# Optimization experiments

Measured on AMD Instinct MI355X. Metric: run time of the kernel, lower is better.

Reference implementation:

```python
import jax, jax.numpy as jnp
import numpy as np

P = 2        # patch size (all 3 dims)
NB = 8       # num_bands
N = 16       # d_state
DTR = 8      # dt_rank = d_model // 16
DCONV = 4    # d_conv
SMAX = 2.0   # smax_dt = smax_B = smax_C


def _ln(x, g, b):
    mu = x.mean(-1, keepdims=True)
    v = ((x - mu) ** 2).mean(-1, keepdims=True)
    return (x - mu) / jnp.sqrt(v + 1e-5) * g + b


def _silu(x):
    return x * jax.nn.sigmoid(x)


def _ssm_layer(x, band, m, rho, Win, bin_, convw, convb, Wx, Wdt, bdt, Alog, Dp,
               Wout, bout, edt, eB, eC, wr, wm):
    # x: [B, L, d_model] -> bidirectional conditioned selective scan (BiFCSSM)
    Bsz, L, _ = x.shape
    ED = convw.shape[0]
    xz = x @ Win + bin_
    xp, z = xz[..., :ED], xz[..., ED:]
    # depthwise causal conv1d over L
    xpad = jnp.pad(xp, ((0, 0), (DCONV - 1, 0), (0, 0)))
    xc = sum(xpad[:, k:k + L, :] * convw[:, k] for k in range(DCONV)) + convb
    xc = _silu(xc)
    dbl = xc @ Wx                                    # [B,L,DTR+2N]
    dt = jax.nn.softplus(dbl[..., :DTR] @ Wdt + bdt)  # [B,L,ED]
    # band/radius/mask conditioned modulation of delta, B, C
    s_dt = SMAX * jax.nn.sigmoid(edt[band][None] + wr[0] * rho[None] + wm[0] * m)
    s_B = SMAX * jax.nn.sigmoid(eB[band][None] + wr[1] * rho[None] + wm[1] * m)
    s_C = SMAX * jax.nn.sigmoid(eC[band][None] + wr[2] * rho[None] + wm[2] * m)
    dt = dt * s_dt[..., None]
    Bm = dbl[..., DTR:DTR + N] * s_B[..., None]       # [B,L,N]
    Cm = dbl[..., DTR + N:] * s_C[..., None]          # [B,L,N]
    A = -jnp.exp(Alog)                                # [ED,N]
    dA = jnp.exp(dt[..., None] * A)                   # [B,L,ED,N]
    dBu = (dA - 1.0) / A * Bm[:, :, None, :] * xc[..., None]   # exact ZOH
    dA_s = jnp.moveaxis(dA, 1, 0)
    dBu_s = jnp.moveaxis(dBu, 1, 0)
    C_s = jnp.moveaxis(Cm, 1, 0)
    h0 = jnp.zeros((Bsz, ED, N), x.dtype)

    def step(h, inp):
        a, bu, c = inp
        h = a * h + bu
        return h, jnp.einsum('ben,bn->be', h, c)

    _, yf = jax.lax.scan(step, h0, (dA_s, dBu_s, C_s))
    _, yb = jax.lax.scan(step, h0, (dA_s, dBu_s, C_s), reverse=True)
    y = jnp.moveaxis(yf + yb, 0, 1) + Dp * xc
    y = y * _silu(z)
    return y @ Wout + bout


def _fwd(kspace_ri, mask, pe_w, pe_b, pu_w, pu_b, ln_g, ln_b, fn_g, fn_b,
         cond_band, cond_rad_w, cond_mask_w, l0_Win, l0_bin, l0_convw, l0_convb,
         l0_Wx, l0_Wdt, l0_bdt, l0_Alog, l0_D, l0_Wout, l0_bout, l0_edt, l0_eB,
         l0_eC, l0_wr, l0_wm):
    Bsz, C, nx, ny, nz = kspace_ri.shape
    gx, gy, gz = nx // P, ny // P, nz // P
    L = gx * gy * gz
    # patch embed (Conv3d, kernel==stride) as blocked einsum
    xr = kspace_ri.reshape(Bsz, C, gx, P, gy, P, gz, P)
    x = jnp.einsum('bcxiyjzk,dcijk->bdxyz', xr, pe_w) + pe_b[None, :, None, None, None]
    DM = x.shape[1]
    x = x.reshape(Bsz, DM, L).transpose(0, 2, 1)               # [B,L,D]
    m = mask.reshape(Bsz, 1, gx, P, gy, P, gz, P).mean(axis=(3, 5, 7)).reshape(Bsz, L)
    m = jnp.clip(m, 0.0, 1.0)
    # raster scan ordering: identity permutation, rho_bar, band ids
    rho = jnp.arange(L, dtype=x.dtype) / float(L - 1)
    band = jnp.clip(jnp.floor(rho * NB).astype(jnp.int32), 0, NB - 1)
    # condition tokens
    cond = cond_band[band][None] + rho[None, :, None] * cond_rad_w + m[:, :, None] * cond_mask_w
    h = _ln(x + cond, ln_g, ln_b)
    h = h + _ssm_layer(_ln(h, fn_g, fn_b), band, m, rho, l0_Win, l0_bin, l0_convw,
                       l0_convb, l0_Wx, l0_Wdt, l0_bdt, l0_Alog, l0_D, l0_Wout,
                       l0_bout, l0_edt, l0_eB, l0_eC, l0_wr, l0_wm)
    # patch unembed (ConvTranspose3d, kernel==stride) as blocked einsum
    hg = h.transpose(0, 2, 1).reshape(Bsz, DM, gx, gy, gz)
    out = jnp.einsum('bdxyz,dcijk->bcxiyjzk', hg, pu_w).reshape(Bsz, C, nx, ny, nz)
    out = out + pu_b[None, :, None, None, None]
    return kspace_ri + out


def setup_inputs() -> dict:
    key = jax.random.key(0)
    ks = jax.random.split(key, 24)
    ED, DM, CIN = 256, 128, 16

    def nrm(k, shape, s):
        return jax.random.normal(k, shape, jnp.float32) * s

    return {
        'kspace_ri': jax.random.normal(ks[0], (1, CIN, 64, 64, 16), jnp.float32),
        'mask': jax.random.uniform(ks[1], (1, 1, 64, 64, 16), jnp.float32),
        'pe_w': nrm(ks[2], (DM, CIN, P, P, P), 0.09),
        'pe_b': nrm(ks[3], (DM,), 0.02),
        'pu_w': nrm(ks[4], (DM, CIN, P, P, P), 0.05),
        'pu_b': jnp.zeros((CIN,), jnp.float32),
        'ln_g': jnp.ones((DM,), jnp.float32),
        'ln_b': jnp.zeros((DM,), jnp.float32),
        'fn_g': jnp.ones((DM,), jnp.float32),
        'fn_b': jnp.zeros((DM,), jnp.float32),
        'cond_band': nrm(ks[5], (NB, DM), 0.02),
        'cond_rad_w': nrm(ks[6], (DM,), 0.02),
        'cond_mask_w': nrm(ks[7], (DM,), 0.02),
        'l0_Win': nrm(ks[8], (DM, 2 * ED), 0.05),
        'l0_bin': jnp.zeros((2 * ED,), jnp.float32),
        'l0_convw': nrm(ks[9], (ED, DCONV), 0.2),
        'l0_convb': jnp.zeros((ED,), jnp.float32),
        'l0_Wx': nrm(ks[10], (ED, DTR + 2 * N), 0.05),
        'l0_Wdt': nrm(ks[11], (DTR, ED), 0.1),
        'l0_bdt': jnp.full((ED,), -3.0, jnp.float32),
        'l0_Alog': jnp.log(jnp.tile(jnp.arange(1, N + 1, dtype=jnp.float32), (ED, 1))),
        'l0_D': jnp.ones((ED,), jnp.float32),
        'l0_Wout': nrm(ks[12], (ED, DM), 0.05),
        'l0_bout': jnp.zeros((DM,), jnp.float32),
        'l0_edt': nrm(ks[13], (NB,), 0.1),
        'l0_eB': nrm(ks[14], (NB,), 0.1),
        'l0_eC': nrm(ks[15], (NB,), 0.1),
        'l0_wr': nrm(ks[16], (3,), 0.1),
        'l0_wm': nrm(ks[17], (3,), 0.1),
    }


def reference(kspace_ri, mask, pe_w, pe_b, pu_w, pu_b, ln_g, ln_b, fn_g, fn_b,
              cond_band, cond_rad_w, cond_mask_w, l0_Win, l0_bin, l0_convw,
              l0_convb, l0_Wx, l0_Wdt, l0_bdt, l0_Alog, l0_D, l0_Wout, l0_bout,
              l0_edt, l0_eB, l0_eC, l0_wr, l0_wm):
    return _fwd(kspace_ri, mask, pe_w, pe_b, pu_w, pu_b, ln_g, ln_b, fn_g, fn_b,
                cond_band, cond_rad_w, cond_mask_w, l0_Win, l0_bin, l0_convw,
                l0_convb, l0_Wx, l0_Wdt, l0_bdt, l0_Alog, l0_D, l0_Wout, l0_bout,
                l0_edt, l0_eB, l0_eC, l0_wr, l0_wm)
```

## Files before the change

### kernel.cpp

```cpp
#include <hip/hip_runtime.h>
#include <hip/hip_bf16.h>

#define L_TOK 8192
#define NCh 256
#define CLh 32

typedef short bf16x8 __attribute__((ext_vector_type(8)));
typedef float f32x4 __attribute__((ext_vector_type(4)));

static __device__ __forceinline__ ushort f2bf(float x) {
    union { float f; uint u; } v; v.f = x;
    uint r = v.u + 0x7fffu + ((v.u >> 16) & 1u);
    return (ushort)(r >> 16);
}
static __device__ __forceinline__ float bf2f(ushort h) {
    union { float f; uint u; } v; v.u = ((uint)h) << 16;
    return v.f;
}
static __device__ __forceinline__ void f2hl(float x, ushort* hi, ushort* lo) {
    ushort h = f2bf(x);
    *hi = h;
    *lo = f2bf(x - bf2f(h));
}

__global__ __launch_bounds__(256) void maskpool_k(const float* __restrict__ mask, float* __restrict__ m) {
    int l = blockIdx.x * 256 + threadIdx.x;
    int xg = l >> 8, yg = (l >> 3) & 31, zg = l & 7;
    float s = 0.f;
    for (int i2 = 0; i2 < 2; ++i2)
        for (int j2 = 0; j2 < 2; ++j2)
            for (int k2 = 0; k2 < 2; ++k2)
                s += mask[(2 * xg + i2) * 1024 + (2 * yg + j2) * 16 + 2 * zg + k2];
    s *= 0.125f;
    m[l] = fminf(fmaxf(s, 0.f), 1.f);
}

__global__ __launch_bounds__(256) void prep_w(const float* __restrict__ pe_w, const float* __restrict__ Win,
                                              const float* __restrict__ Wx, const float* __restrict__ Wout,
                                              const float* __restrict__ pu_w,
                                              ushort* __restrict__ wH, ushort* __restrict__ wL) {
    int i = blockIdx.x * 256 + threadIdx.x;
    if (i >= 147456) return;
    float v;
    if (i < 16384) {
        v = pe_w[i];
    } else if (i < 81920) {
        int j = i - 16384; int n = j >> 7, k = j & 127;
        v = Win[k * 512 + n];
    } else if (i < 98304) {
        int j = i - 81920; int n = j >> 8, k = j & 255;
        v = (n < 40) ? Wx[k * 40 + n] : 0.f;
    } else if (i < 131072) {
        int j = i - 98304; int n = j >> 8, k = j & 255;
        v = Wout[k * 128 + n];
    } else {
        int j = i - 131072; int n = j >> 7, k = j & 127;
        v = pu_w[k * 128 + n];
    }
    ushort h, lo; f2hl(v, &h, &lo);
    wH[i] = h; wL[i] = lo;
}

__global__ __launch_bounds__(256) void gather_k(const float* __restrict__ ks,
                                                ushort* __restrict__ xH, ushort* __restrict__ xL) {
    int i = blockIdx.x * 256 + threadIdx.x;
    int l = i >> 7, t = i & 127;
    int cc = t >> 3, ijk = t & 7;
    int xg = l >> 8, yg = (l >> 3) & 31, zg = l & 7;
    int i2 = (ijk >> 2) & 1, j2 = (ijk >> 1) & 1, k2 = ijk & 1;
    float v = ks[cc * 65536 + (2 * xg + i2) * 1024 + (2 * yg + j2) * 16 + 2 * zg + k2];
    ushort h, lo; f2hl(v, &h, &lo);
    xH[i] = h; xL[i] = lo;
}

template <int MODE, int K>
__global__ __launch_bounds__(256) void mgemm_k(const ushort* __restrict__ Ah, const ushort* __restrict__ Al,
                                               const ushort* __restrict__ Bh, const ushort* __restrict__ Bl,
                                               float* __restrict__ outF,
                                               ushort* __restrict__ outH, ushort* __restrict__ outL,
                                               const float* __restrict__ p0, const float* __restrict__ p1,
                                               const float* __restrict__ p2, const float* __restrict__ p3,
                                               const float* __restrict__ p4) {
    __shared__ ushort AsH[128][72], AsL[128][72];
    __shared__ ushort BsH[64][72], BsL[64][72];
    const int tid = threadIdx.x;
    const int lane = tid & 63, wave = tid >> 6;
    const int wm = wave & 1, wn = wave >> 1;
    const int ln = lane & 15, q = lane >> 4;
    const int mb = blockIdx.x * 128, nb = blockIdx.y * 64;

    f32x4 acc[4][2];
#pragma unroll
    for (int rb = 0; rb < 4; ++rb)
#pragma unroll
        for (int cb = 0; cb < 2; ++cb)
            acc[rb][cb] = (f32x4){0.f, 0.f, 0.f, 0.f};

    for (int kc = 0; kc < K; kc += 64) {
        __syncthreads();
        for (int u = tid; u < 1024; u += 256) {
            int r = u >> 3, g = u & 7;
            size_t go = (size_t)(mb + r) * K + kc + g * 8;
            *(uint4*)&AsH[r][g * 8] = *(const uint4*)&Ah[go];
            *(uint4*)&AsL[r][g * 8] = *(const uint4*)&Al[go];
        }
        for (int u = tid; u < 512; u += 256) {
            int r = u >> 3, g = u & 7;
            size_t go = (size_t)(nb + r) * K + kc + g * 8;
            *(uint4*)&BsH[r][g * 8] = *(const uint4*)&Bh[go];
            *(uint4*)&BsL[r][g * 8] = *(const uint4*)&Bl[go];
        }
        __syncthreads();
#pragma unroll
        for (int ks = 0; ks < 64; ks += 32) {
            const int kk = ks + q * 8;
            bf16x8 ah[4], al[4], bh[2], bl[2];
#pragma unroll
            for (int rb = 0; rb < 4; ++rb) {
                ah[rb] = *(const bf16x8*)&AsH[wm * 64 + rb * 16 + ln][kk];
                al[rb] = *(const bf16x8*)&AsL[wm * 64 + rb * 16 + ln][kk];
            }
#pragma unroll
            for (int cb = 0; cb < 2; ++cb) {
                bh[cb] = *(const bf16x8*)&BsH[wn * 32 + cb * 16 + ln][kk];
                bl[cb] = *(const bf16x8*)&BsL[wn * 32 + cb * 16 + ln][kk];
            }
#pragma unroll
            for (int rb = 0; rb < 4; ++rb)
#pragma unroll
                for (int cb = 0; cb < 2; ++cb) {
                    acc[rb][cb] = __builtin_amdgcn_mfma_f32_16x16x32_bf16(ah[rb], bh[cb], acc[rb][cb], 0, 0, 0);
                    acc[rb][cb] = __builtin_amdgcn_mfma_f32_16x16x32_bf16(ah[rb], bl[cb], acc[rb][cb], 0, 0, 0);
                    acc[rb][cb] = __builtin_amdgcn_mfma_f32_16x16x32_bf16(al[rb], bh[cb], acc[rb][cb], 0, 0, 0);
                }
        }
    }

#pragma unroll
    for (int rb = 0; rb < 4; ++rb) {
#pragma unroll
        for (int cb = 0; cb < 2; ++cb) {
#pragma unroll
            for (int r = 0; r < 4; ++r) {
                int l = mb + wm * 64 + rb * 16 + q * 4 + r;
                int col = nb + wn * 32 + cb * 16 + ln;
                float v = acc[rb][cb][r];
                if (MODE == 0) {
                    float rho = (float)l * (1.0f / 8191.0f);
                    int band = min(7, (int)(rho * 8.0f));
                    outF[(size_t)l * 128 + col] =
                        v + p0[col] + p1[band * 128 + col] + rho * p2[col] + p4[l] * p3[col];
                } else if (MODE == 1) {
                    outF[(size_t)l * 512 + col] = v + p0[col];
                } else if (MODE == 2) {
                    float o = v + p0[col] + p1[(size_t)l * 128 + col];
                    ushort h, lo; f2hl(o, &h, &lo);
                    outH[(size_t)l * 128 + col] = h;
                    outL[(size_t)l * 128 + col] = lo;
                } else if (MODE == 3) {
                    int xg = l >> 8, yg = (l >> 3) & 31, zg = l & 7;
                    int c = col >> 3, ijk = col & 7;
                    int i2 = (ijk >> 2) & 1, j2 = (ijk >> 1) & 1, k2 = ijk & 1;
                    size_t idx = (size_t)((c * 64 + 2 * xg + i2) * 64 + (2 * yg + j2)) * 16 + 2 * zg + k2;
                    outF[idx] = v + p0[c] + p1[idx];
                } else {
                    if (col < 40) outF[(size_t)l * 40 + col] = v;
                }
            }
        }
    }
}

__global__ __launch_bounds__(128) void ln2_k(const float* __restrict__ x,
                                             const float* __restrict__ ln_g, const float* __restrict__ ln_b,
                                             const float* __restrict__ fn_g, const float* __restrict__ fn_b,
                                             float* __restrict__ h,
                                             ushort* __restrict__ hnH, ushort* __restrict__ hnL) {
    int l = blockIdx.x, d = threadIdx.x;
    __shared__ float red[4];
    float v = x[(size_t)l * 128 + d];
    float s = v, s2 = v * v;
#pragma unroll
    for (int o = 32; o > 0; o >>= 1) { s += __shfl_xor(s, o, 64); s2 += __shfl_xor(s2, o, 64); }
    if ((d & 63) == 0) { red[d >> 6] = s; red[2 + (d >> 6)] = s2; }
    __syncthreads();
    float S = red[0] + red[1], S2 = red[2] + red[3];
    float mu = S * (1.f / 128.f);
    float var = S2 * (1.f / 128.f) - mu * mu;
    float rstd = rsqrtf(fmaxf(var, 0.f) + 1e-5f);
    float hv = (v - mu) * rstd * ln_g[d] + ln_b[d];
    h[(size_t)l * 128 + d] = hv;
    __syncthreads();
    s = hv; s2 = hv * hv;
#pragma unroll
    for (int o = 32; o > 0; o >>= 1) { s += __shfl_xor(s, o, 64); s2 += __shfl_xor(s2, o, 64); }
    if ((d & 63) == 0) { red[d >> 6] = s; red[2 + (d >> 6)] = s2; }
    __syncthreads();
    S = red[0] + red[1]; S2 = red[2] + red[3];
    mu = S * (1.f / 128.f);
    var = S2 * (1.f / 128.f) - mu * mu;
    rstd = rsqrtf(fmaxf(var, 0.f) + 1e-5f);
    float o2 = (hv - mu) * rstd * fn_g[d] + fn_b[d];
    ushort hh, ll; f2hl(o2, &hh, &ll);
    hnH[(size_t)l * 128 + d] = hh;
    hnL[(size_t)l * 128 + d] = ll;
}

__global__ __launch_bounds__(256) void conv_k(const float* __restrict__ xz, const float* __restrict__ convw,
                                              const float* __restrict__ convb, float* __restrict__ xc,
                                              ushort* __restrict__ xcH, ushort* __restrict__ xcL) {
    int l = blockIdx.x, e = threadIdx.x;
    float acc = convb[e];
#pragma unroll
    for (int k = 0; k < 4; ++k) {
        int lp = l - 3 + k;
        if (lp >= 0) acc += xz[(size_t)lp * 512 + e] * convw[e * 4 + k];
    }
    float sg = 1.f / (1.f + expf(-acc));
    float v = acc * sg;
    xc[(size_t)l * 256 + e] = v;
    ushort h, lo; f2hl(v, &h, &lo);
    xcH[(size_t)l * 256 + e] = h;
    xcL[(size_t)l * 256 + e] = lo;
}

__global__ __launch_bounds__(256) void dtk_k(const float* __restrict__ dbl, const float* __restrict__ Wdt,
                                             const float* __restrict__ bdt, const float* __restrict__ m,
                                             const float* __restrict__ edt, const float* __restrict__ eB,
                                             const float* __restrict__ eC, const float* __restrict__ wr,
                                             const float* __restrict__ wm,
                                             float* __restrict__ dt, float* __restrict__ Bmo, float* __restrict__ Cmo) {
    int l = blockIdx.x, e = threadIdx.x;
    __shared__ float ds[40];
    __shared__ float sc[3];
    if (e < 40) ds[e] = dbl[(size_t)l * 40 + e];
    if (e == 0) {
        float rho = (float)l * (1.0f / 8191.0f);
        int band = min(7, (int)(rho * 8.0f));
        float mv = m[l];
        sc[0] = 2.0f / (1.f + expf(-(edt[band] + wr[0] * rho + wm[0] * mv)));
        sc[1] = 2.0f / (1.f + expf(-(eB[band] + wr[1] * rho + wm[1] * mv)));
        sc[2] = 2.0f / (1.f + expf(-(eC[band] + wr[2] * rho + wm[2] * mv)));
    }
    __syncthreads();
    float acc = bdt[e];
#pragma unroll
    for (int r = 0; r < 8; ++r) acc += ds[r] * Wdt[r * 256 + e];
    float sp = (acc > 20.f) ? acc : log1pf(expf(acc));
    dt[(size_t)l * 256 + e] = sp * sc[0];
    if (e < 16) Bmo[(size_t)l * 16 + e] = ds[8 + e] * sc[1];
    else if (e < 32) Cmo[(size_t)l * 16 + (e - 16)] = ds[24 + (e - 16)] * sc[2];
}

template <int PHASE>
__global__ __launch_bounds__(256) void scan_k(const float* __restrict__ dt, const float* __restrict__ xc,
                                              const float* __restrict__ Bm, const float* __restrict__ Cm,
                                              const float* __restrict__ Alog,
                                              float* __restrict__ Hb, float* __restrict__ sdtb,
                                              float* __restrict__ yf, float* __restrict__ yb) {
    const int c = blockIdx.x, dir = blockIdx.y, e = threadIdx.x;
    __shared__ float bms[CLh][16];
    __shared__ float cms[CLh][16];
    for (int idx = e; idx < CLh * 16; idx += 256) {
        bms[idx >> 4][idx & 15] = Bm[c * (CLh * 16) + idx];
        if (PHASE == 1) cms[idx >> 4][idx & 15] = Cm[c * (CLh * 16) + idx];
    }
    float A2[16], iv[16], h[16];
#pragma unroll
    for (int n = 0; n < 16; ++n) {
        float ea = expf(Alog[e * 16 + n]);
        A2[n] = -ea * 1.44269504088896f;
        iv[n] = -1.0f / ea;
    }
    const size_t hofs = (size_t)(dir * NCh + c) * 4096 + e * 16;
// ... 57 lines not shown
                                                 const float* __restrict__ Alog) {
    int id = blockIdx.x * 256 + threadIdx.x;
    int dir = id >> 12, en = id & 4095, e = en >> 4;
    float A2 = -expf(Alog[en]) * 1.44269504088896f;
    float hi = 0.f;
    for (int g = 0; g < NCh / 8; ++g) {
        float Pv[8], qv[8];
#pragma unroll
        for (int j = 0; j < 8; ++j) {
            int c = dir ? (NCh - 1 - (g * 8 + j)) : (g * 8 + j);
            Pv[j] = sdtb[c * 256 + e];
            qv[j] = Hb[(size_t)(dir * NCh + c) * 4096 + en];
        }
#pragma unroll
        for (int j = 0; j < 8; ++j) {
            int c = dir ? (NCh - 1 - (g * 8 + j)) : (g * 8 + j);
            float P = exp2f(A2 * Pv[j]);
            Hb[(size_t)(dir * NCh + c) * 4096 + en] = hi;
            hi = P * hi + qv[j];
        }
    }
}

__global__ __launch_bounds__(256) void gate_k(const float* __restrict__ yf, const float* __restrict__ yb,
                                              const float* __restrict__ xc, const float* __restrict__ xz,
                                              const float* __restrict__ Dp,
                                              ushort* __restrict__ yH, ushort* __restrict__ yL) {
    int i = blockIdx.x * 256 + threadIdx.x;
    int e = i & 255, l = i >> 8;
    float zv = xz[(size_t)l * 512 + 256 + e];
    float yv = yf[i] + yb[i] + Dp[e] * xc[i];
    float v = yv * (zv / (1.f + expf(-zv)));
    ushort h, lo; f2hl(v, &h, &lo);
    yH[i] = h; yL[i] = lo;
}

extern "C" void kernel_launch(void* const* d_in, const int* in_sizes, int n_in,
                              void* d_out, int out_size, void* d_ws, size_t ws_size,
                              hipStream_t stream) {
    const float* ks    = (const float*)d_in[0];
    const float* mask  = (const float*)d_in[1];
    const float* pe_w  = (const float*)d_in[2];
    const float* pe_b  = (const float*)d_in[3];
    const float* pu_w  = (const float*)d_in[4];
    const float* pu_b  = (const float*)d_in[5];
    const float* ln_g  = (const float*)d_in[6];
    const float* ln_b  = (const float*)d_in[7];
    const float* fn_g  = (const float*)d_in[8];
    const float* fn_b  = (const float*)d_in[9];
    const float* cond_band = (const float*)d_in[10];
    const float* cond_rad  = (const float*)d_in[11];
    const float* cond_mask = (const float*)d_in[12];
    const float* Win   = (const float*)d_in[13];
    const float* bin_  = (const float*)d_in[14];
    const float* convw = (const float*)d_in[15];
    const float* convb = (const float*)d_in[16];
    const float* Wx    = (const float*)d_in[17];
    const float* Wdt   = (const float*)d_in[18];
    const float* bdt   = (const float*)d_in[19];
    const float* Alog  = (const float*)d_in[20];
    const float* Dp    = (const float*)d_in[21];
    const float* Wout  = (const float*)d_in[22];
    const float* bout  = (const float*)d_in[23];
    const float* edt   = (const float*)d_in[24];
    const float* eB    = (const float*)d_in[25];
    const float* eC    = (const float*)d_in[26];
    const float* wr    = (const float*)d_in[27];
    const float* wm    = (const float*)d_in[28];
    float* out = (float*)d_out;

    char* base = (char*)d_ws;
    size_t o = 0;
    auto alloc = [&](size_t bytes) { char* p = base + o; o += (bytes + 255) & ~(size_t)255; return p; };
    float*  mbuf = (float*)alloc(32768);
    ushort* wH   = (ushort*)alloc(294912);
    ushort* wL   = (ushort*)alloc(294912);
    ushort* xinH = (ushort*)alloc(2097152);
    ushort* xinL = (ushort*)alloc(2097152);
    float*  x    = (float*)alloc(4194304);
    float*  h_   = (float*)alloc(4194304);
    ushort* hnH  = (ushort*)alloc(2097152);
    ushort* hnL  = (ushort*)alloc(2097152);
    float*  xz   = (float*)alloc(16777216);
    float*  xc   = (float*)alloc(8388608);
    ushort* xcH  = (ushort*)alloc(4194304);
    ushort* xcL  = (ushort*)alloc(4194304);
    float*  dbl  = (float*)alloc(1310720);
    float*  dt   = (float*)alloc(8388608);
    float*  Bm   = (float*)alloc(524288);
    float*  Cm   = (float*)alloc(524288);
    float*  Hb   = (float*)alloc(8388608);
    float*  sdtb = (float*)alloc(262144);
    float*  yf   = (float*)alloc(8388608);
    float*  yb   = (float*)alloc(8388608);
    ushort* yH   = (ushort*)alloc(4194304);
    ushort* yL   = (ushort*)alloc(4194304);
    ushort* hfH  = (ushort*)alloc(2097152);
    ushort* hfL  = (ushort*)alloc(2097152);

    maskpool_k<<<32, 256, 0, stream>>>(mask, mbuf);
    prep_w<<<576, 256, 0, stream>>>(pe_w, Win, Wx, Wout, pu_w, wH, wL);
    gather_k<<<4096, 256, 0, stream>>>(ks, xinH, xinL);
    mgemm_k<0, 128><<<dim3(64, 2), 256, 0, stream>>>(xinH, xinL, wH, wL, x, nullptr, nullptr,
                                                     pe_b, cond_band, cond_rad, cond_mask, mbuf);
    ln2_k<<<8192, 128, 0, stream>>>(x, ln_g, ln_b, fn_g, fn_b, h_, hnH, hnL);
    mgemm_k<1, 128><<<dim3(64, 8), 256, 0, stream>>>(hnH, hnL, wH + 16384, wL + 16384, xz, nullptr, nullptr,
                                                     bin_, nullptr, nullptr, nullptr, nullptr);
    conv_k<<<8192, 256, 0, stream>>>(xz, convw, convb, xc, xcH, xcL);
    mgemm_k<4, 256><<<dim3(64, 1), 256, 0, stream>>>(xcH, xcL, wH + 81920, wL + 81920, dbl, nullptr, nullptr,
                                                     nullptr, nullptr, nullptr, nullptr, nullptr);
    dtk_k<<<8192, 256, 0, stream>>>(dbl, Wdt, bdt, mbuf, edt, eB, eC, wr, wm, dt, Bm, Cm);
    scan_k<0><<<dim3(NCh, 2), 256, 0, stream>>>(dt, xc, Bm, Cm, Alog, Hb, sdtb, nullptr, nullptr);
    combine_k<<<32, 256, 0, stream>>>(Hb, sdtb, Alog);
    scan_k<1><<<dim3(NCh, 2), 256, 0, stream>>>(dt, xc, Bm, Cm, Alog, Hb, sdtb, yf, yb);
    gate_k<<<8192, 256, 0, stream>>>(yf, yb, xc, xz, Dp, yH, yL);
    mgemm_k<2, 256><<<dim3(64, 2), 256, 0, stream>>>(yH, yL, wH + 98304, wL + 98304, nullptr, hfH, hfL,
                                                     bout, h_, nullptr, nullptr, nullptr);
    mgemm_k<3, 128><<<dim3(64, 2), 256, 0, stream>>>(hfH, hfL, wH + 131072, wL + 131072, out, nullptr, nullptr,
                                                     pu_b, ks, nullptr, nullptr, nullptr);
}
```

Baseline: 295.4 us.

## Fuse pipeline kernels: embed+LN, Wx·Wdt folding, gate into Wout GEMM

Restructures most of the pipeline. The mask pooling and weight prep are merged into one launch. The gather, embed GEMM and double LayerNorm become one kernel. The in-projection epilogue now splits out x and silu(z). Wx and Wdt are folded offline into a single projection weight, so dt comes straight from one GEMM, and the gate is fused into the Wout GEMM's A-loading. The aim is to cut launches and intermediate global round-trips (xz, dbl, gather/gate buffers). In exchange it adds extra rounding from precomputing Wx·Wdt and more complex per-kernel code.

After: 281.3 us. -4.7%, faster.

```diff
diff --git a/kernel.cpp b/kernel.cpp
--- a/kernel.cpp
+++ b/kernel.cpp
@@ -23,64 +23,199 @@
     *lo = f2bf(x - bf2f(h));
 }
 
-__global__ __launch_bounds__(256) void maskpool_k(const float* __restrict__ mask, float* __restrict__ m) {
-    int l = blockIdx.x * 256 + threadIdx.x;
-    int xg = l >> 8, yg = (l >> 3) & 31, zg = l & 7;
-    float s = 0.f;
-    for (int i2 = 0; i2 < 2; ++i2)
-        for (int j2 = 0; j2 < 2; ++j2)
-            for (int k2 = 0; k2 < 2; ++k2)
-                s += mask[(2 * xg + i2) * 1024 + (2 * yg + j2) * 16 + 2 * zg + k2];
-    s *= 0.125f;
-    m[l] = fminf(fmaxf(s, 0.f), 1.f);
-}
-
-__global__ __launch_bounds__(256) void prep_w(const float* __restrict__ pe_w, const float* __restrict__ Win,
-                                              const float* __restrict__ Wx, const float* __restrict__ Wout,
-                                              const float* __restrict__ pu_w,
-                                              ushort* __restrict__ wH, ushort* __restrict__ wL) {
-    int i = blockIdx.x * 256 + threadIdx.x;
-    if (i >= 147456) return;
+#define W_PE   0
+#define W_WIN  16384
+#define W_WOUT 81920
+#define W_PU   114688
+#define W_PROJ 131072
+#define W_TOT  212992
+
+__global__ __launch_bounds__(256) void prep_k(const float* __restrict__ pe_w, const float* __restrict__ Win,
+                                              const float* __restrict__ Wx, const float* __restrict__ Wdt,
+                                              const float* __restrict__ Wout, const float* __restrict__ pu_w,
+                                              const float* __restrict__ mask,
+                                              ushort* __restrict__ wH, ushort* __restrict__ wL,
+                                              float* __restrict__ mbuf) {
+    int b = blockIdx.x;
+    if (b >= 832) {
+        int l = (b - 832) * 256 + threadIdx.x;
+        int xg = l >> 8, yg = (l >> 3) & 31, zg = l & 7;
+        float s = 0.f;
+        for (int i2 = 0; i2 < 2; ++i2)
+            for (int j2 = 0; j2 < 2; ++j2)
+                for (int k2 = 0; k2 < 2; ++k2)
+                    s += mask[(2 * xg + i2) * 1024 + (2 * yg + j2) * 16 + 2 * zg + k2];
+        s *= 0.125f;
+        mbuf[l] = fminf(fmaxf(s, 0.f), 1.f);
+        return;
+    }
+    int i = b * 256 + threadIdx.x;
     float v;
     if (i < 16384) {
         v = pe_w[i];
     } else if (i < 81920) {
         int j = i - 16384; int n = j >> 7, k = j & 127;
         v = Win[k * 512 + n];
-    } else if (i < 98304) {
+    } else if (i < 114688) {
         int j = i - 81920; int n = j >> 8, k = j & 255;
-        v = (n < 40) ? Wx[k * 40 + n] : 0.f;
+        v = Wout[k * 128 + n];
     } else if (i < 131072) {
-        int j = i - 98304; int n = j >> 8, k = j & 255;
-        v = Wout[k * 128 + n];
+        int j = i - 114688; int n = j >> 7, k = j & 127;
+        v = pu_w[k * 128 + n];
     } else {
-        int j = i - 131072; int n = j >> 7, k = j & 127;
-        v = pu_w[k * 128 + n];
+        int j = i - 131072; int n = j >> 8, k = j & 255;
+        if (n < 256) {
+            float s = 0.f;
+#pragma unroll
+            for (int r = 0; r < 8; ++r) s += Wx[k * 40 + r] * Wdt[r * 256 + n];
+            v = s;
+        } else if (n < 288) {
+            v = Wx[k * 40 + 8 + (n - 256)];
+        } else {
+            v = 0.f;
+        }
     }
     ushort h, lo; f2hl(v, &h, &lo);
     wH[i] = h; wL[i] = lo;
 }
 
-__global__ __launch_bounds__(256) void gather_k(const float* __restrict__ ks,
-                                                ushort* __restrict__ xH, ushort* __restrict__ xL) {
-    int i = blockIdx.x * 256 + threadIdx.x;
-    int l = i >> 7, t = i & 127;
-    int cc = t >> 3, ijk = t & 7;
-    int xg = l >> 8, yg = (l >> 3) & 31, zg = l & 7;
-    int i2 = (ijk >> 2) & 1, j2 = (ijk >> 1) & 1, k2 = ijk & 1;
-    float v = ks[cc * 65536 + (2 * xg + i2) * 1024 + (2 * yg + j2) * 16 + 2 * zg + k2];
-    ushort h, lo; f2hl(v, &h, &lo);
-    xH[i] = h; xL[i] = lo;
-}
-
-template <int MODE, int K>
-__global__ __launch_bounds__(256) void mgemm_k(const ushort* __restrict__ Ah, const ushort* __restrict__ Al,
-                                               const ushort* __restrict__ Bh, const ushort* __restrict__ Bl,
-                                               float* __restrict__ outF,
-                                               ushort* __restrict__ outH, ushort* __restrict__ outL,
-                                               const float* __restrict__ p0, const float* __restrict__ p1,
-                                               const float* __restrict__ p2, const float* __restrict__ p3,
-                                               const float* __restrict__ p4) {
+__global__ __launch_bounds__(256) void embed_ln_k(const float* __restrict__ ks,
+                                                  const ushort* __restrict__ wH, const ushort* __restrict__ wL,
+                                                  const float* __restrict__ pe_b, const float* __restrict__ cond_band,
+                                                  const float* __restrict__ cond_rad, const float* __restrict__ cond_mask,
+                                                  const float* __restrict__ mbuf,
+                                                  const float* __restrict__ ln_g, const float* __restrict__ ln_b,
+                                                  const float* __restrict__ fn_g, const float* __restrict__ fn_b,
+                                                  float* __restrict__ h_,
+                                                  ushort* __restrict__ hnH, ushort* __restrict__ hnL) {
+    __shared__ __align__(16) char smem[46080];
+    ushort (*AsH)[72] = (ushort(*)[72])(smem);
+    ushort (*AsL)[72] = (ushort(*)[72])(smem + 4608);
+    ushort (*BsH)[72] = (ushort(*)[72])(smem + 9216);
+    ushort (*BsL)[72] = (ushort(*)[72])(smem + 27648);
+    float  (*Cs)[132] = (float(*)[132])(smem);
+
+    const int tid = threadIdx.x;
+    const int lane = tid & 63, wn = tid >> 6;
+    const int ln = lane & 15, q = lane >> 4;
+    const int mb = blockIdx.x * 32;
+
+    f32x4 acc[2][2];
+#pragma unroll
+    for (int rb = 0; rb < 2; ++rb)
+#pragma unroll
+        for (int cb = 0; cb < 2; ++cb) acc[rb][cb] = (f32x4){0.f, 0.f, 0.f, 0.f};
+
+    for (int kc = 0; kc < 128; kc += 64) {
+        __syncthreads();
+        for (int u = tid; u < 2048; u += 256) {
+            int r = u >> 6, kk = u & 63;
+            int l = mb + r, k = kc + kk;
+            int cc = k >> 3, ijk = k & 7;
+            int xg = l >> 8, yg = (l >> 3) & 31, zg = l & 7;
+            int i2 = (ijk >> 2) & 1, j2 = (ijk >> 1) & 1, k2 = ijk & 1;
+            float v = ks[cc * 65536 + (2 * xg + i2) * 1024 + (2 * yg + j2) * 16 + 2 * zg + k2];
+            ushort h, lo; f2hl(v, &h, &lo);
+            AsH[r][kk] = h; AsL[r][kk] = lo;
+        }
+        for (int u = tid; u < 1024; u += 256) {
+            int n = u >> 3, g = u & 7;
+            *(uint4*)&BsH[n][g * 8] = *(const uint4*)&wH[W_PE + n * 128 + kc + g * 8];
+            *(uint4*)&BsL[n][g * 8] = *(const uint4*)&wL[W_PE + n * 128 + kc + g * 8];
+        }
+        __syncthreads();
+#pragma unroll
+        for (int ks_ = 0; ks_ < 64; ks_ += 32) {
+            const int kk = ks_ + q * 8;
+            bf16x8 ah[2], al[2], bh[2], bl[2];
+#pragma unroll
+            for (int rb = 0; rb < 2; ++rb) {
+                ah[rb] = *(const bf16x8*)&AsH[rb * 16 + ln][kk];
+                al[rb] = *(const bf16x8*)&AsL[rb * 16 + ln][kk];
+            }
+#pragma unroll
+            for (int cb = 0; cb < 2; ++cb) {
+                bh[cb] = *(const bf16x8*)&BsH[wn * 32 + cb * 16 + ln][kk];
+                bl[cb] = *(const bf16x8*)&BsL[wn * 32 + cb * 16 + ln][kk];
+            }
+#pragma unroll
+            for (int rb = 0; rb < 2; ++rb)
+#pragma unroll
+                for (int cb = 0; cb < 2; ++cb) {
+                    acc[rb][cb] = __builtin_amdgcn_mfma_f32_16x16x32_bf16(ah[rb], bh[cb], acc[rb][cb], 0, 0, 0);
+                    acc[rb][cb] = __builtin_amdgcn_mfma_f32_16x16x32_bf16(ah[rb], bl[cb], acc[rb][cb], 0, 0, 0);
+                    acc[rb][cb] = __builtin_amdgcn_mfma_f32_16x16x32_bf16(al[rb], bh[cb], acc[rb][cb], 0, 0, 0);
+                }
+        }
+    }
+    __syncthreads();
+#pragma unroll
+    for (int rb = 0; rb < 2; ++rb) {
+#pragma unroll
+        for (int cb = 0; cb < 2; ++cb) {
+#pragma unroll
+            for (int r = 0; r < 4; ++r) {
+                int row = rb * 16 + q * 4 + r;
+                int col = wn * 32 + cb * 16 + ln;
+                int l = mb + row;
+                float rho = (float)l * (1.0f / 8191.0f);
+                int band = min(7, (int)(rho * 8.0f));
+                Cs[row][col] = acc[rb][cb][r] + pe_b[col] + cond_band[band * 128 + col]
+                               + rho * cond_rad[col] + mbuf[l] * cond_mask[col];
+            }
+        }
+    }
+    __syncthreads();
+    {
+        int row = tid >> 3, j = tid & 7;
+        int l = mb + row;
+        float v16[16];
+        float s = 0.f, s2 = 0.f;
+#pragma unroll
+        for (int i = 0; i < 16; ++i) {
+            float v = Cs[row][j * 16 + i];
+            v16[i] = v; s += v; s2 += v * v;
+        }
+#pragma unroll
+        for (int o = 1; o < 8; o <<= 1) { s += __shfl_xor(s, o, 8); s2 += __shfl_xor(s2, o, 8); }
+        float mu = s * (1.f / 128.f);
+        float var = s2 * (1.f / 128.f) - mu * mu;
+        float rstd = rsqrtf(fmaxf(var, 0.f) + 1e-5f);
+        float hv[16];
+        s = 0.f; s2 = 0.f;
+#pragma unroll
+        for (int i = 0; i < 16; ++i) {
+            int col = j * 16 + i;
+            float h = (v16[i] - mu) * rstd * ln_g[col] + ln_b[col];
+            hv[i] = h; s += h; s2 += h * h;
+        }
+#pragma unroll
+        for (int i = 0; i < 16; i += 4)
+            *(float4*)&h_[(size_t)l * 128 + j * 16 + i] = make_float4(hv[i], hv[i + 1], hv[i + 2], hv[i + 3]);
+#pragma unroll
+        for (int o = 1; o < 8; o <<= 1) { s += __shfl_xor(s, o, 8); s2 += __shfl_xor(s2, o, 8); }
+        mu = s * (1.f / 128.f);
+        var = s2 * (1.f / 128.f) - mu * mu;
+        rstd = rsqrtf(fmaxf(var, 0.f) + 1e-5f);
+        union { ushort u[16]; uint4 v4[2]; } oh, ol;
+#pragma unroll
+        for (int i = 0; i < 16; ++i) {
+            int col = j * 16 + i;
+            float o2 = (hv[i] - mu) * rstd * fn_g[col] + fn_b[col];
+            ushort hh, ll; f2hl(o2, &hh, &ll);
+            oh.u[i] = hh; ol.u[i] = ll;
+        }
+        *(uint4*)&hnH[(size_t)l * 128 + j * 16] = oh.v4[0];
+        *(uint4*)&hnH[(size_t)l * 128 + j * 16 + 8] = oh.v4[1];
+        *(uint4*)&hnL[(size_t)l * 128 + j * 16] = ol.v4[0];
+        *(uint4*)&hnL[(size_t)l * 128 + j * 16 + 8] = ol.v4[1];
+    }
+}
+
+__global__ __launch_bounds__(256) void win_k(const ushort* __restrict__ Ah, const ushort* __restrict__ Al,
+                                             const ushort* __restrict__ wH, const ushort* __restrict__ wL,
+                                             const float* __restrict__ bin_,
+                                             float* __restrict__ xp, float* __restrict__ sz) {
     __shared__ ushort AsH[128][72], AsL[128][72];
     __shared__ ushort BsH[64][72], BsL[64][72];
     const int tid = threadIdx.x;
@@ -93,27 +228,26 @@
 #pragma unroll
     for (int rb = 0; rb < 4; ++rb)
 #pragma unroll
-        for (int cb = 0; cb < 2; ++cb)
-            acc[rb][cb] = (f32x4){0.f, 0.f, 0.f, 0.f};
-
-    for (int kc = 0; kc < K; kc += 64) {
+        for (int cb = 0; cb < 2; ++cb) acc[rb][cb] = (f32x4){0.f, 0.f, 0.f, 0.f};
+
+    for (int kc = 0; kc < 128; kc += 64) {
         __syncthreads();
         for (int u = tid; u < 1024; u += 256) {
             int r = u >> 3, g = u & 7;
-            size_t go = (size_t)(mb + r) * K + kc + g * 8;
+            size_t go = (size_t)(mb + r) * 128 + kc + g * 8;
             *(uint4*)&AsH[r][g * 8] = *(const uint4*)&Ah[go];
             *(uint4*)&AsL[r][g * 8] = *(const uint4*)&Al[go];
         }
         for (int u = tid; u < 512; u += 256) {
-            int r = u >> 3, g = u & 7;
-            size_t go = (size_t)(nb + r) * K + kc + g * 8;
-            *(uint4*)&BsH[r][g * 8] = *(const uint4*)&Bh[go];
-            *(uint4*)&BsL[r][g * 8] = *(const uint4*)&Bl[go];
-        }
-        __syncthreads();
-#pragma unroll
-        for (int ks = 0; ks < 64; ks += 32) {
-            const int kk = ks + q * 8;
+            int n = u >> 3, g = u & 7;
+            size_t go = (size_t)(W_WIN) + (size_t)(nb + n) * 128 + kc + g * 8;
+            *(uint4*)&BsH[n][g * 8] = *(const uint4*)&wH[go];
+            *(uint4*)&BsL[n][g * 8] = *(const uint4*)&wL[go];
+        }
+        __syncthreads();
+#pragma unroll
+        for (int ks_ = 0; ks_ < 64; ks_ += 32) {
+            const int kk = ks_ + q * 8;
             bf16x8 ah[4], al[4], bh[2], bl[2];
 #pragma unroll
             for (int rb = 0; rb < 4; ++rb) {
@@ -135,121 +269,139 @@
                 }
         }
     }
-
-#pragma unroll
-    for (int rb = 0; rb < 4; ++rb) {
-#pragma unroll
-        for (int cb = 0; cb < 2; ++cb) {
+#pragma unroll
+    for (int rb = 0; rb < 4; ++rb)
+#pragma unroll
+        for (int cb = 0; cb < 2; ++cb)
 #pragma unroll
             for (int r = 0; r < 4; ++r) {
                 int l = mb + wm * 64 + rb * 16 + q * 4 + r;
                 int col = nb + wn * 32 + cb * 16 + ln;
-                float v = acc[rb][cb][r];
-                if (MODE == 0) {
-                    float rho = (float)l * (1.0f / 8191.0f);
-                    int band = min(7, (int)(rho * 8.0f));
-                    outF[(size_t)l * 128 + col] =
-                        v + p0[col] + p1[band * 128 + col] + rho * p2[col] + p4[l] * p3[col];
-                } else if (MODE == 1) {
-                    outF[(size_t)l * 512 + col] = v + p0[col];
-                } else if (MODE == 2) {
-                    float o = v + p0[col] + p1[(size_t)l * 128 + col];
-                    ushort h, lo; f2hl(o, &h, &lo);
-                    outH[(size_t)l * 128 + col] = h;
-                    outL[(size_t)l * 128 + col] = lo;
-                } else if (MODE == 3) {
-                    int xg = l >> 8, yg = (l >> 3) & 31, zg = l & 7;
-                    int c = col >> 3, ijk = col & 7;
-                    int i2 = (ijk >> 2) & 1, j2 = (ijk >> 1) & 1, k2 = ijk & 1;
-                    size_t idx = (size_t)((c * 64 + 2 * xg + i2) * 64 + (2 * yg + j2)) * 16 + 2 * zg + k2;
-                    outF[idx] = v + p0[c] + p1[idx];
+                float v = acc[rb][cb][r] + bin_[col];
+                if (col < 256) {
+                    xp[(size_t)l * 256 + col] = v;
                 } else {
-                    if (col < 40) outF[(size_t)l * 40 + col] = v;
+                    sz[(size_t)l * 256 + (col - 256)] = v / (1.f + expf(-v));
                 }
             }
-        }
-    }
-}
-
-__global__ __launch_bounds__(128) void ln2_k(const float* __restrict__ x,
-                                             const float* __restrict__ ln_g, const float* __restrict__ ln_b,
-                                             const float* __restrict__ fn_g, const float* __restrict__ fn_b,
-                                             float* __restrict__ h,
-                                             ushort* __restrict__ hnH, ushort* __restrict__ hnL) {
-    int l = blockIdx.x, d = threadIdx.x;
-    __shared__ float red[4];
-    float v = x[(size_t)l * 128 + d];
-    float s = v, s2 = v * v;
-#pragma unroll
-    for (int o = 32; o > 0; o >>= 1) { s += __shfl_xor(s, o, 64); s2 += __shfl_xor(s2, o, 64); }
-    if ((d & 63) == 0) { red[d >> 6] = s; red[2 + (d >> 6)] = s2; }
-    __syncthreads();
-    float S = red[0] + red[1], S2 = red[2] + red[3];
-    float mu = S * (1.f / 128.f);
-    float var = S2 * (1.f / 128.f) - mu * mu;
-    float rstd = rsqrtf(fmaxf(var, 0.f) + 1e-5f);
-    float hv = (v - mu) * rstd * ln_g[d] + ln_b[d];
-    h[(size_t)l * 128 + d] = hv;
-    __syncthreads();
-    s = hv; s2 = hv * hv;
-#pragma unroll
-    for (int o = 32; o > 0; o >>= 1) { s += __shfl_xor(s, o, 64); s2 += __shfl_xor(s2, o, 64); }
-    if ((d & 63) == 0) { red[d >> 6] = s; red[2 + (d >> 6)] = s2; }
-    __syncthreads();
-    S = red[0] + red[1]; S2 = red[2] + red[3];
-    mu = S * (1.f / 128.f);
-    var = S2 * (1.f / 128.f) - mu * mu;
-    rstd = rsqrtf(fmaxf(var, 0.f) + 1e-5f);
-    float o2 = (hv - mu) * rstd * fn_g[d] + fn_b[d];
-    ushort hh, ll; f2hl(o2, &hh, &ll);
-    hnH[(size_t)l * 128 + d] = hh;
-    hnL[(size_t)l * 128 + d] = ll;
-}
-
-__global__ __launch_bounds__(256) void conv_k(const float* __restrict__ xz, const float* __restrict__ convw,
-                                              const float* __restrict__ convb, float* __restrict__ xc,
-                                              ushort* __restrict__ xcH, ushort* __restrict__ xcL) {
-    int l = blockIdx.x, e = threadIdx.x;
-    float acc = convb[e];
+}
+
+__global__ __launch_bounds__(256) void conv_k(const float* __restrict__ xp, const float* __restrict__ convw,
+                                              const float* __restrict__ convb, float* __restrict__ xc) {
+    int id = blockIdx.x * 256 + threadIdx.x;
+    int l = id >> 6, e4 = (id & 63) * 4;
+    float4 cw[4];
+#pragma unroll
+    for (int j = 0; j < 4; ++j) cw[j] = *(const float4*)&convw[(e4 + j) * 4];
+    float4 cb = *(const float4*)&convb[e4];
+    float o[4] = {cb.x, cb.y, cb.z, cb.w};
 #pragma unroll
     for (int k = 0; k < 4; ++k) {
         int lp = l - 3 + k;
-        if (lp >= 0) acc += xz[(size_t)lp * 512 + e] * convw[e * 4 + k];
-    }
-    float sg = 1.f / (1.f + expf(-acc));
-    float v = acc * sg;
-    xc[(size_t)l * 256 + e] = v;
-    ushort h, lo; f2hl(v, &h, &lo);
-    xcH[(size_t)l * 256 + e] = h;
-    xcL[(size_t)l * 256 + e] = lo;
-}
-
-__global__ __launch_bounds__(256) void dtk_k(const float* __restrict__ dbl, const float* __restrict__ Wdt,
-                                             const float* __restrict__ bdt, const float* __restrict__ m,
-                                             const float* __restrict__ edt, const float* __restrict__ eB,
-                                             const float* __restrict__ eC, const float* __restrict__ wr,
-                                             const float* __restrict__ wm,
-                                             float* __restrict__ dt, float* __restrict__ Bmo, float* __restrict__ Cmo) {
-    int l = blockIdx.x, e = threadIdx.x;
-    __shared__ float ds[40];
-    __shared__ float sc[3];
-    if (e < 40) ds[e] = dbl[(size_t)l * 40 + e];
-    if (e == 0) {
-        float rho = (float)l * (1.0f / 8191.0f);
-        int band = min(7, (int)(rho * 8.0f));
-        float mv = m[l];
-        sc[0] = 2.0f / (1.f + expf(-(edt[band] + wr[0] * rho + wm[0] * mv)));
-        sc[1] = 2.0f / (1.f + expf(-(eB[band] + wr[1] * rho + wm[1] * mv)));
-        sc[2] = 2.0f / (1.f + expf(-(eC[band] + wr[2] * rho + wm[2] * mv)));
-    }
-    __syncthreads();
-    float acc = bdt[e];
-#pragma unroll
-    for (int r = 0; r < 8; ++r) acc += ds[r] * Wdt[r * 256 + e];
-    float sp = (acc > 20.f) ? acc : log1pf(expf(acc));
-    dt[(size_t)l * 256 + e] = sp * sc[0];
-    if (e < 16) Bmo[(size_t)l * 16 + e] = ds[8 + e] * sc[1];
-    else if (e < 32) Cmo[(size_t)l * 16 + (e - 16)] = ds[24 + (e - 16)] * sc[2];
+        if (lp >= 0) {
+            float4 t = *(const float4*)&xp[(size_t)lp * 256 + e4];
+            o[0] += t.x * ((const float*)&cw[0])[k];
+            o[1] += t.y * ((const float*)&cw[1])[k];
+            o[2] += t.z * ((const float*)&cw[2])[k];
+            o[3] += t.w * ((const float*)&cw[3])[k];
+        }
+    }
+    float4 r;
+    r.x = o[0] / (1.f + expf(-o[0]));
+    r.y = o[1] / (1.f + expf(-o[1]));
+    r.z = o[2] / (1.f + expf(-o[2]));
+    r.w = o[3] / (1.f + expf(-o[3]));
+    *(float4*)&xc[(size_t)l * 256 + e4] = r;
+}
+
+__global__ __launch_bounds__(256) void proj_k(const float* __restrict__ xc,
+                                              const ushort* __restrict__ wH, const ushort* __restrict__ wL,
+                                              const float* __restrict__ bdt, const float* __restrict__ mbuf,
+                                              const float* __restrict__ edt, const float* __restrict__ eB,
+                                              const float* __restrict__ eC, const float* __restrict__ wr,
+                                              const float* __restrict__ wm,
+                                              float* __restrict__ dt, float* __restrict__ Bm, float* __restrict__ Cm) {
+    __shared__ ushort AsH[128][72], AsL[128][72];
+    __shared__ ushort BsH[64][72], BsL[64][72];
+    const int tid = threadIdx.x;
+    const int lane = tid & 63, wave = tid >> 6;
+    const int wm_ = wave & 1, wn = wave >> 1;
+    const int ln = lane & 15, q = lane >> 4;
+    const int mb = blockIdx.x * 128, nb = blockIdx.y * 64;
+
+    f32x4 acc[4][2];
+#pragma unroll
+    for (int rb = 0; rb < 4; ++rb)
+#pragma unroll
+        for (int cb = 0; cb < 2; ++cb) acc[rb][cb] = (f32x4){0.f, 0.f, 0.f, 0.f};
+
+    for (int kc = 0; kc < 256; kc += 64) {
+        __syncthreads();
+        for (int u = tid; u < 2048; u += 256) {
+            int r = u >> 4, kq = u & 15;
+            float4 v = *(const float4*)&xc[(size_t)(mb + r) * 256 + kc + kq * 4];
+            union { ushort u[4]; uint2 v2; } hh, ll;
+            f2hl(v.x, &hh.u[0], &ll.u[0]); f2hl(v.y, &hh.u[1], &ll.u[1]);
+            f2hl(v.z, &hh.u[2], &ll.u[2]); f2hl(v.w, &hh.u[3], &ll.u[3]);
+            *(uint2*)&AsH[r][kq * 4] = hh.v2;
+            *(uint2*)&AsL[r][kq * 4] = ll.v2;
+        }
+        for (int u = tid; u < 512; u += 256) {
+            int n = u >> 3, g = u & 7;
+            size_t go = (size_t)(W_PROJ) + (size_t)(nb + n) * 256 + kc + g * 8;
+            *(uint4*)&BsH[n][g * 8] = *(const uint4*)&wH[go];
+            *(uint4*)&BsL[n][g * 8] = *(const uint4*)&wL[go];
+        }
+        __syncthreads();
+#pragma unroll
+        for (int ks_ = 0; ks_ < 64; ks_ += 32) {
+            const int kk = ks_ + q * 8;
+            bf16x8 ah[4], al[4], bh[2], bl[2];
+#pragma unroll
+            for (int rb = 0; rb < 4; ++rb) {
+                ah[rb] = *(const bf16x8*)&AsH[wm_ * 64 + rb * 16 + ln][kk];
+                al[rb] = *(const bf16x8*)&AsL[wm_ * 64 + rb * 16 + ln][kk];
+            }
+#pragma unroll
+            for (int cb = 0; cb < 2; ++cb) {
+                bh[cb] = *(const bf16x8*)&BsH[wn * 32 + cb * 16 + ln][kk];
+                bl[cb] = *(const bf16x8*)&BsL[wn * 32 + cb * 16 + ln][kk];
+            }
+#pragma unroll
+            for (int rb = 0; rb < 4; ++rb)
+#pragma unroll
+                for (int cb = 0; cb < 2; ++cb) {
+                    acc[rb][cb] = __builtin_amdgcn_mfma_f32_16x16x32_bf16(ah[rb], bh[cb], acc[rb][cb], 0, 0, 0);
+                    acc[rb][cb] = __builtin_amdgcn_mfma_f32_16x16x32_bf16(ah[rb], bl[cb], acc[rb][cb], 0, 0, 0);
+                    acc[rb][cb] = __builtin_amdgcn_mfma_f32_16x16x32_bf16(al[rb], bh[cb], acc[rb][cb], 0, 0, 0);
+                }
+        }
+    }
+#pragma unroll
+    for (int rb = 0; rb < 4; ++rb)
+#pragma unroll
+        for (int cb = 0; cb < 2; ++cb)
+#pragma unroll
+            for (int r = 0; r < 4; ++r) {
+                int l = mb + wm_ * 64 + rb * 16 + q * 4 + r;
+                int col = nb + wn * 32 + cb * 16 + ln;
+                float v = acc[rb][cb][r];
+                float rho = (float)l * (1.0f / 8191.0f);
+                int band = min(7, (int)(rho * 8.0f));
+                float mv = mbuf[l];
+                if (col < 256) {
+                    float sc0 = 2.0f / (1.f + expf(-(edt[band] + wr[0] * rho + wm[0] * mv)));
+                    float v2 = v + bdt[col];
+                    float sp = (v2 > 20.f) ? v2 : log1pf(expf(v2));
+                    dt[(size_t)l * 256 + col] = sp * sc0;
+                } else if (col < 272) {
+                    float sc1 = 2.0f / (1.f + expf(-(eB[band] + wr[1] * rho + wm[1] * mv)));
+                    Bm[(size_t)l * 16 + (col - 256)] = v * sc1;
+                } else if (col < 288) {
+                    float sc2 = 2.0f / (1.f + expf(-(eC[band] + wr[2] * rho + wm[2] * mv)));
+                    Cm[(size_t)l * 16 + (col - 272)] = v * sc2;
+                }
+            }
 }
 
 template <int PHASE>
@@ -353,17 +505,163 @@
     }
 }
 
-__global__ __launch_bounds__(256) void gate_k(const float* __restrict__ yf, const float* __restrict__ yb,
-                                              const float* __restrict__ xc, const float* __restrict__ xz,
+__global__ __launch_bounds__(256) void wout_k(const float* __restrict__ yf, const float* __restrict__ yb,
+                                              const float* __restrict__ xc, const float* __restrict__ sz,
                                               const float* __restrict__ Dp,
-                                              ushort* __restrict__ yH, ushort* __restrict__ yL) {
-    int i = blockIdx.x * 256 + threadIdx.x;
-    int e = i & 255, l = i >> 8;
-    float zv = xz[(size_t)l * 512 + 256 + e];
-    float yv = yf[i] + yb[i] + Dp[e] * xc[i];
-    float v = yv * (zv / (1.f + expf(-zv)));
-    ushort h, lo; f2hl(v, &h, &lo);
-    yH[i] = h; yL[i] = lo;
+                                              const ushort* __restrict__ wH, const ushort* __restrict__ wL,
+                                              const float* __restrict__ bout, const float* __restrict__ h_,
+                                              ushort* __restrict__ hfH, ushort* __restrict__ hfL) {
+    __shared__ ushort AsH[64][72], AsL[64][72];
+    __shared__ ushort BsH[64][72], BsL[64][72];
+    const int tid = threadIdx.x;
+    const int lane = tid & 63, wave = tid >> 6;
+    const int wm = wave & 1, wn = wave >> 1;
+    const int ln = lane & 15, q = lane >> 4;
+    const int mb = blockIdx.x * 64, nb = blockIdx.y * 64;
+
+    f32x4 acc[2][2];
+#pragma unroll
+    for (int rb = 0; rb < 2; ++rb)
+#pragma unroll
+        for (int cb = 0; cb < 2; ++cb) acc[rb][cb] = (f32x4){0.f, 0.f, 0.f, 0.f};
+
+    for (int kc = 0; kc < 256; kc += 64) {
+        __syncthreads();
+        for (int u = tid; u < 1024; u += 256) {
+            int r = u >> 4, kq = u & 15;
+            size_t go = (size_t)(mb + r) * 256 + kc + kq * 4;
+            float4 a = *(const float4*)&yf[go];
+            float4 b = *(const float4*)&yb[go];
+            float4 x = *(const float4*)&xc[go];
+            float4 s = *(const float4*)&sz[go];
+            float4 d = *(const float4*)&Dp[kc + kq * 4];
+            float v0 = (a.x + b.x + d.x * x.x) * s.x;
+            float v1 = (a.y + b.y + d.y * x.y) * s.y;
+            float v2 = (a.z + b.z + d.z * x.z) * s.z;
+            float v3 = (a.w + b.w + d.w * x.w) * s.w;
+            union { ushort u[4]; uint2 v2; } hh, ll;
+            f2hl(v0, &hh.u[0], &ll.u[0]); f2hl(v1, &hh.u[1], &ll.u[1]);
+            f2hl(v2, &hh.u[2], &ll.u[2]); f2hl(v3, &hh.u[3], &ll.u[3]);
+            *(uint2*)&AsH[r][kq * 4] = hh.v2;
+            *(uint2*)&AsL[r][kq * 4] = ll.v2;
+        }
+        for (int u = tid; u < 512; u += 256) {
+            int n = u >> 3, g = u & 7;
+            size_t go = (size_t)(W_WOUT) + (size_t)(nb + n) * 256 + kc + g * 8;
+            *(uint4*)&BsH[n][g * 8] = *(const uint4*)&wH[go];
+            *(uint4*)&BsL[n][g * 8] = *(const uint4*)&wL[go];
+        }
+        __syncthreads();
+#pragma unroll
+        for (int ks_ = 0; ks_ < 64; ks_ += 32) {
+            const int kk = ks_ + q * 8;
+            bf16x8 ah[2], al[2], bh[2], bl[2];
+#pragma unroll
+            for (int rb = 0; rb < 2; ++rb) {
+                ah[rb] = *(const bf16x8*)&AsH[wm * 32 + rb * 16 + ln][kk];
+                al[rb] = *(const bf16x8*)&AsL[wm * 32 + rb * 16 + ln][kk];
+            }
+#pragma unroll
+            for (int cb = 0; cb < 2; ++cb) {
+                bh[cb] = *(const bf16x8*)&BsH[wn * 32 + cb * 16 + ln][kk];
+                bl[cb] = *(const bf16x8*)&BsL[wn * 32 + cb * 16 + ln][kk];
+            }
+#pragma unroll
+            for (int rb = 0; rb < 2; ++rb)
+#pragma unroll
+                for (int cb = 0; cb < 2; ++cb) {
+                    acc[rb][cb] = __builtin_amdgcn_mfma_f32_16x16x32_bf16(ah[rb], bh[cb], acc[rb][cb], 0, 0, 0);
+                    acc[rb][cb] = __builtin_amdgcn_mfma_f32_16x16x32_bf16(ah[rb], bl[cb], acc[rb][cb], 0, 0, 0);
+                    acc[rb][cb] = __builtin_amdgcn_mfma_f32_16x16x32_bf16(al[rb], bh[cb], acc[rb][cb], 0, 0, 0);
+                }
+        }
+    }
+#pragma unroll
+    for (int rb = 0; rb < 2; ++rb)
+#pragma unroll
+        for (int cb = 0; cb < 2; ++cb)
+#pragma unroll
+            for (int r = 0; r < 4; ++r) {
+                int l = mb + wm * 32 + rb * 16 + q * 4 + r;
+                int col = nb + wn * 32 + cb * 16 + ln;
+                float v = acc[rb][cb][r] + bout[col] + h_[(size_t)l * 128 + col];
+                ushort hh, ll; f2hl(v, &hh, &ll);
+                hfH[(size_t)l * 128 + col] = hh;
+                hfL[(size_t)l * 128 + col] = ll;
+            }
+}
+
+__global__ __launch_bounds__(256) void unembed_k(const ushort* __restrict__ Ah, const ushort* __restrict__ Al,
+                                                 const ushort* __restrict__ wH, const ushort* __restrict__ wL,
+                                                 const float* __restrict__ pu_b, const float* __restrict__ ks,
+                                                 float* __restrict__ out) {
+    __shared__ ushort AsH[64][72], AsL[64][72];
+    __shared__ ushort BsH[64][72], BsL[64][72];
+    const int tid = threadIdx.x;
+    const int lane = tid & 63, wave = tid >> 6;
+    const int wm = wave & 1, wn = wave >> 1;
+    const int ln = lane & 15, q = lane >> 4;
+    const int mb = blockIdx.x * 64, nb = blockIdx.y * 64;
+
+    f32x4 acc[2][2];
+#pragma unroll
+    for (int rb = 0; rb < 2; ++rb)
+#pragma unroll
+        for (int cb = 0; cb < 2; ++cb) acc[rb][cb] = (f32x4){0.f, 0.f, 0.f, 0.f};
+
+    for (int kc = 0; kc < 128; kc += 64) {
+        __syncthreads();
+        for (int u = tid; u < 512; u += 256) {
+            int r = u >> 3, g = u & 7;
+            size_t go = (size_t)(mb + r) * 128 + kc + g * 8;
+            *(uint4*)&AsH[r][g * 8] = *(const uint4*)&Ah[go];
+            *(uint4*)&AsL[r][g * 8] = *(const uint4*)&Al[go];
+        }
+        for (int u = tid; u < 512; u += 256) {
+            int n = u >> 3, g = u & 7;
+            size_t go = (size_t)(W_PU) + (size_t)(nb + n) * 128 + kc + g * 8;
+            *(uint4*)&BsH[n][g * 8] = *(const uint4*)&wH[go];
+            *(uint4*)&BsL[n][g * 8] = *(const uint4*)&wL[go];
+        }
+        __syncthreads();
+#pragma unroll
+        for (int ks_ = 0; ks_ < 64; ks_ += 32) {
+            const int kk = ks_ + q * 8;
+            bf16x8 ah[2], al[2], bh[2], bl[2];
+#pragma unroll
+            for (int rb = 0; rb < 2; ++rb) {
+                ah[rb] = *(const bf16x8*)&AsH[wm * 32 + rb * 16 + ln][kk];
+                al[rb] = *(const bf16x8*)&AsL[wm * 32 + rb * 16 + ln][kk];
+            }
+#pragma unroll
+            for (int cb = 0; cb < 2; ++cb) {
+                bh[cb] = *(const bf16x8*)&BsH[wn * 32 + cb * 16 + ln][kk];
+                bl[cb] = *(const bf16x8*)&BsL[wn * 32 + cb * 16 + ln][kk];
+            }
+#pragma unroll
+            for (int rb = 0; rb < 2; ++rb)
+#pragma unroll
+                for (int cb = 0; cb < 2; ++cb) {
+                    acc[rb][cb] = __builtin_amdgcn_mfma_f32_16x16x32_bf16(ah[rb], bh[cb], acc[rb][cb], 0, 0, 0);
+                    acc[rb][cb] = __builtin_amdgcn_mfma_f32_16x16x32_bf16(ah[rb], bl[cb], acc[rb][cb], 0, 0, 0);
+                    acc[rb][cb] = __builtin_amdgcn_mfma_f32_16x16x32_bf16(al[rb], bh[cb], acc[rb][cb], 0, 0, 0);
+                }
+        }
+    }
+#pragma unroll
+    for (int rb = 0; rb < 2; ++rb)
+#pragma unroll
+        for (int cb = 0; cb < 2; ++cb)
+#pragma unroll
+            for (int r = 0; r < 4; ++r) {
+                int l = mb + wm * 32 + rb * 16 + q * 4 + r;
+                int col = nb + wn * 32 + cb * 16 + ln;
+                int xg = l >> 8, yg = (l >> 3) & 31, zg = l & 7;
+                int c = col >> 3, ijk = col & 7;
+                int i2 = (ijk >> 2) & 1, j2 = (ijk >> 1) & 1, k2 = ijk & 1;
+                size_t idx = (size_t)((c * 64 + 2 * xg + i2) * 64 + (2 * yg + j2)) * 16 + 2 * zg + k2;
+                out[idx] = acc[rb][cb][r] + pu_b[c] + ks[idx];
+            }
 }
 
 extern "C" void kernel_launch(void* const* d_in, const int* in_sizes, int n_in,
@@ -404,19 +702,14 @@
     size_t o = 0;
     auto alloc = [&](size_t bytes) { char* p = base + o; o += (bytes + 255) & ~(size_t)255; return p; };
     float*  mbuf = (float*)alloc(32768);
-    ushort* wH   = (ushort*)alloc(294912);
-    ushort* wL   = (ushort*)alloc(294912);
-    ushort* xinH = (ushort*)alloc(2097152);
-    ushort* xinL = (ushort*)alloc(2097152);
-    float*  x    = (float*)alloc(4194304);
+    ushort* wH   = (ushort*)alloc(W_TOT * 2);
+    ushort* wL   = (ushort*)alloc(W_TOT * 2);
     float*  h_   = (float*)alloc(4194304);
     ushort* hnH  = (ushort*)alloc(2097152);
     ushort* hnL  = (ushort*)alloc(2097152);
-    float*  xz   = (float*)alloc(16777216);
+    float*  xp   = (float*)alloc(8388608);
+    float*  sz   = (float*)alloc(8388608);
     float*  xc   = (float*)alloc(8388608);
-    ushort* xcH  = (ushort*)alloc(4194304);
-    ushort* xcL  = (ushort*)alloc(4194304);
-    float*  dbl  = (float*)alloc(1310720);
     float*  dt   = (float*)alloc(8388608);
     float*  Bm   = (float*)alloc(524288);
     float*  Cm   = (float*)alloc(524288);
@@ -424,29 +717,18 @@
     float*  sdtb = (float*)alloc(262144);
     float*  yf   = (float*)alloc(8388608);
     float*  yb   = (float*)alloc(8388608);
-    ushort* yH   = (ushort*)alloc(4194304);
-    ushort* yL   = (ushort*)alloc(4194304);
     ushort* hfH  = (ushort*)alloc(2097152);
     ushort* hfL  = (ushort*)alloc(2097152);
 
-    maskpool_k<<<32, 256, 0, stream>>>(mask, mbuf);
-    prep_w<<<576, 256, 0, stream>>>(pe_w, Win, Wx, Wout, pu_w, wH, wL);
-    gather_k<<<4096, 256, 0, stream>>>(ks, xinH, xinL);
-    mgemm_k<0, 128><<<dim3(64, 2), 256, 0, stream>>>(xinH, xinL, wH, wL, x, nullptr, nullptr,
-                                                     pe_b, cond_band, cond_rad, cond_mask, mbuf);
-    ln2_k<<<8192, 128, 0, stream>>>(x, ln_g, ln_b, fn_g, fn_b, h_, hnH, hnL);
-    mgemm_k<1, 128><<<dim3(64, 8), 256, 0, stream>>>(hnH, hnL, wH + 16384, wL + 16384, xz, nullptr, nullptr,
-                                                     bin_, nullptr, nullptr, nullptr, nullptr);
-    conv_k<<<8192, 256, 0, stream>>>(xz, convw, convb, xc, xcH, xcL);
-    mgemm_k<4, 256><<<dim3(64, 1), 256, 0, stream>>>(xcH, xcL, wH + 81920, wL + 81920, dbl, nullptr, nullptr,
-                                                     nullptr, nullptr, nullptr, nullptr, nullptr);
-    dtk_k<<<8192, 256, 0, stream>>>(dbl, Wdt, bdt, mbuf, edt, eB, eC, wr, wm, dt, Bm, Cm);
+    prep_k<<<864, 256, 0, stream>>>(pe_w, Win, Wx, Wdt, Wout, pu_w, mask, wH, wL, mbuf);
+    embed_ln_k<<<256, 256, 0, stream>>>(ks, wH, wL, pe_b, cond_band, cond_rad, cond_mask, mbuf,
+                                        ln_g, ln_b, fn_g, fn_b, h_, hnH, hnL);
+    win_k<<<dim3(64, 8), 256, 0, stream>>>(hnH, hnL, wH, wL, bin_, xp, sz);
+    conv_k<<<2048, 256, 0, stream>>>(xp, convw, convb, xc);
+    proj_k<<<dim3(64, 5), 256, 0, stream>>>(xc, wH, wL, bdt, mbuf, edt, eB, eC, wr, wm, dt, Bm, Cm);
     scan_k<0><<<dim3(NCh, 2), 256, 0, stream>>>(dt, xc, Bm, Cm, Alog, Hb, sdtb, nullptr, nullptr);
     combine_k<<<32, 256, 0, stream>>>(Hb, sdtb, Alog);
     scan_k<1><<<dim3(NCh, 2), 256, 0, stream>>>(dt, xc, Bm, Cm, Alog, Hb, sdtb, yf, yb);
-    gate_k<<<8192, 256, 0, stream>>>(yf, yb, xc, xz, Dp, yH, yL);
-    mgemm_k<2, 256><<<dim3(64, 2), 256, 0, stream>>>(yH, yL, wH + 98304, wL + 98304, nullptr, hfH, hfL,
-                                                     bout, h_, nullptr, nullptr, nullptr);
-    mgemm_k<3, 128><<<dim3(64, 2), 256, 0, stream>>>(hfH, hfL, wH + 131072, wL + 131072, out, nullptr, nullptr,
-                                                     pu_b, ks, nullptr, nullptr, nullptr);
-}
+    wout_k<<<dim3(128, 2), 256, 0, stream>>>(yf, yb, xc, sz, Dp, wH, wL, bout, h_, hfH, hfL);
+    unembed_k<<<dim3(128, 2), 256, 0, stream>>>(hfH, hfL, wH, wL, pu_b, ks, out);
+}
```
